# Kernel optimization log

Measured on AMD Instinct MI355X. Metric: run time of the kernel, lower is better.

The kernel has to match this reference:

```python
import jax, jax.numpy as jnp
import numpy as np

N_NODES = 100000
N_EDGES = 3200000
D_FEAT = 512
HIDDEN = 16
N_CLASSES = 7


def _gcn_conv(x, W, b, src, dst, n_nodes):
    """PyG GCNConv (add_self_loops=True, normalize=True):
    out = D^{-1/2} (A + I) D^{-1/2} X W + b, aggregated at target nodes (dst).
    src/dst already include self loops."""
    h = x @ W  # [N, out_dim] -- transform before scatter (small message dim)
    ones = jnp.ones(dst.shape[0], dtype=x.dtype)
    deg = jax.ops.segment_sum(ones, dst, num_segments=n_nodes)  # in-degree incl. self loop
    dinv = jnp.where(deg > 0, jax.lax.rsqrt(deg), 0.0)
    norm = dinv[src] * dinv[dst]  # [E_tot]
    msg = h[src] * norm[:, None]  # gather + scale
    out = jax.ops.segment_sum(msg, dst, num_segments=n_nodes)  # scatter-add
    return out + b


def setup_inputs() -> dict:
    key = jax.random.key(0)
    k1, k2, k3, k4 = jax.random.split(key, 4)
    x = jax.random.normal(k1, (N_NODES, D_FEAT), dtype=jnp.float32)
    edge_index = jax.random.randint(k2, (2, N_EDGES), 0, N_NODES, dtype=jnp.int64)
    # Glorot-ish init for weights
    W1 = jax.random.normal(k3, (D_FEAT, HIDDEN), dtype=jnp.float32) / np.sqrt(D_FEAT)
    b1 = jnp.zeros((HIDDEN,), dtype=jnp.float32)
    W2 = jax.random.normal(k4, (HIDDEN, N_CLASSES), dtype=jnp.float32) / np.sqrt(HIDDEN)
    b2 = jnp.zeros((N_CLASSES,), dtype=jnp.float32)
    return {"x": x, "edge_index": edge_index, "W1": W1, "b1": b1, "W2": W2, "b2": b2}


def reference(x, edge_index, W1, b1, W2, b2):
    n = x.shape[0]
    loop = jnp.arange(n, dtype=edge_index.dtype)
    src = jnp.concatenate([edge_index[0], loop])  # add self loops (fixed shape)
    dst = jnp.concatenate([edge_index[1], loop])
    h = _gcn_conv(x, W1, b1, src, dst, n)
    h = jax.nn.relu(h)
    # F.dropout(training=self.training): identity in eval/inference baseline
    h = _gcn_conv(h, W2, b2, src, dst, n)
    return jax.nn.log_softmax(h, axis=1)
```

## Files before the change

### kernel.cpp

```cpp
#include <hip/hip_runtime.h>

#define NN 100000
#define NE 3200000
#define DF 512
#define HID 16
#define NC 7
#define NBK 782
#define BCAP 6144
#define GEMM_BLOCKS 1563
#define SC_B 256

__global__ void k_zero_i(int* __restrict__ p, int n) {
    int i = blockIdx.x * blockDim.x + threadIdx.x;
    if (i < n) p[i] = 0;
}

__global__ __launch_bounds__(256) void k_fused(const float* __restrict__ x,
                                               const float* __restrict__ W1,
                                               const int* __restrict__ src,
                                               const int* __restrict__ dst,
                                               float* __restrict__ h1,
                                               int* __restrict__ bcnt,
                                               int* __restrict__ pk) {
    __shared__ float w[DF * HID];
    if (blockIdx.x >= GEMM_BLOCKS) {
        int* hist = (int*)w;
        int* cur  = hist + NBK;
        int b = blockIdx.x - GEMM_BLOCKS;
        const int per = (NE + SC_B - 1) / SC_B;
        int e0 = b * per;
        int e1 = min(e0 + per, NE);
        int tid = threadIdx.x;
        for (int i = tid; i < NBK; i += 256) hist[i] = 0;
        __syncthreads();
        for (int e = e0 + tid; e < e1; e += 256) atomicAdd(&hist[dst[e] >> 7], 1);
        __syncthreads();
        for (int i = tid; i < NBK; i += 256) cur[i] = atomicAdd(&bcnt[i], hist[i]);
        __syncthreads();
        for (int e = e0 + tid; e < e1; e += 256) {
            int d = dst[e];
            int bk = d >> 7;
            int pos = atomicAdd(&cur[bk], 1);
            if (pos < BCAP) pk[(size_t)bk * BCAP + pos] = src[e] | ((d & 127) << 17);
        }
        return;
    }
    {
        const float4* wg = (const float4*)W1;
        float4* wl = (float4*)w;
#pragma unroll
        for (int i = 0; i < 8; ++i) wl[threadIdx.x + 256 * i] = wg[threadIdx.x + 256 * i];
    }
    __syncthreads();
    int wid = (blockIdx.x * 256 + threadIdx.x) >> 6;
    int lane = threadIdx.x & 63;
    int r = lane >> 2, cc = lane & 3;
    int row = wid * 16 + r;
    if (row >= NN) return;
    const float4* xr = (const float4*)(x + (size_t)row * DF);
    const float4* wl = (const float4*)w;
    float4 acc = make_float4(0.f, 0.f, 0.f, 0.f);
#pragma unroll 4
    for (int i = 0; i < DF / 4; ++i) {
        float4 xv = xr[i];
        float4 w0 = wl[(4 * i + 0) * 4 + cc];
        float4 w1v = wl[(4 * i + 1) * 4 + cc];
        float4 w2 = wl[(4 * i + 2) * 4 + cc];
        float4 w3 = wl[(4 * i + 3) * 4 + cc];
        acc.x = fmaf(xv.x, w0.x, fmaf(xv.y, w1v.x, fmaf(xv.z, w2.x, fmaf(xv.w, w3.x, acc.x))));
        acc.y = fmaf(xv.x, w0.y, fmaf(xv.y, w1v.y, fmaf(xv.z, w2.y, fmaf(xv.w, w3.y, acc.y))));
        acc.z = fmaf(xv.x, w0.z, fmaf(xv.y, w1v.z, fmaf(xv.z, w2.z, fmaf(xv.w, w3.z, acc.z))));
        acc.w = fmaf(xv.x, w0.w, fmaf(xv.y, w1v.w, fmaf(xv.z, w2.w, fmaf(xv.w, w3.w, acc.w))));
    }
    *(float4*)(h1 + (size_t)row * HID + cc * 4) = acc;
}

__global__ __launch_bounds__(256) void k_sortB(const int* __restrict__ bcnt,
                                               int* __restrict__ pk,
                                               float* __restrict__ dinv,
                                               float* __restrict__ h1,
                                               int* __restrict__ ptrg,
                                               int* __restrict__ cntg) {
    __shared__ int sorted[BCAP];
    __shared__ int hist[128];
    __shared__ int off[128];
    __shared__ int cur[128];
    __shared__ float dl[128];
    int b = blockIdx.x, tid = threadIdx.x;
    if (tid < 128) hist[tid] = 0;
    __syncthreads();
    int n = min(bcnt[b], BCAP);
    int* p = pk + (size_t)b * BCAP;
    for (int i = tid; i < n; i += 256) atomicAdd(&hist[p[i] >> 17], 1);
    __syncthreads();
    if (tid < 128) off[tid] = hist[tid];
    __syncthreads();
    for (int s2 = 1; s2 < 128; s2 <<= 1) {
        int u = 0;
        if (tid < 128 && tid >= s2) u = off[tid - s2];
        __syncthreads();
        if (tid < 128) off[tid] += u;
        __syncthreads();
    }
    if (tid < 128) {
        int start = off[tid] - hist[tid];
        cur[tid] = start;
        int node = b * 128 + tid;
        float di = rsqrtf((float)hist[tid] + 1.0f);
        dl[tid] = di;
        if (node < NN) {
            dinv[node] = di;
            ptrg[node] = b * BCAP + start;
            cntg[node] = hist[tid];
        }
    }
    __syncthreads();
    for (int i = tid; i < n; i += 256) {
        int v = p[i];
        int pos = atomicAdd(&cur[v >> 17], 1);
        sorted[pos] = v & 0x1FFFF;
    }
    __syncthreads();
    for (int i = tid; i < n; i += 256) p[i] = sorted[i];
    float4* hp = (float4*)(h1 + (size_t)b * 128 * HID);
    for (int i = tid; i < 512; i += 256) {
        int ln = i >> 2;
        int node = b * 128 + ln;
        if (node < NN) {
            float di = dl[ln];
            float4 v = hp[i];
            v.x *= di; v.y *= di; v.z *= di; v.w *= di;
            hp[i] = v;
        }
    }
}

__global__ __launch_bounds__(256) void k_agg1(const int* __restrict__ ptrg,
                                              const int* __restrict__ cntg,
                                              const int* __restrict__ csr,
                                              const float* __restrict__ dinv,
                                              const float* __restrict__ h1s,
                                              const float* __restrict__ b1,
                                              const float* __restrict__ W2,
                                              float* __restrict__ h2s) {
    int tid = threadIdx.x;
    int ch = tid & 15;
    int d = blockIdx.x * 16 + (tid >> 4);
    if (d >= NN) return;
    int st = ptrg[d], n = cntg[d];
    float did = dinv[d];
    float a0 = 0.f, a1 = 0.f;
    int e = st, end = st + n;
    for (; e + 1 < end; e += 2) {
        int s0 = csr[e], s1 = csr[e + 1];
        a0 += h1s[(size_t)s0 * HID + ch];
        a1 += h1s[(size_t)s1 * HID + ch];
    }
    if (e < end) a0 += h1s[(size_t)csr[e] * HID + ch];
    float acc = (a0 + a1 + h1s[(size_t)d * HID + ch]) * did + b1[ch];
    float hr = fmaxf(acc, 0.f);
    float hj = 0.f;
#pragma unroll
    for (int k = 0; k < HID; ++k) {
        float hk = __shfl(hr, k, 16);
        if (ch < NC) hj = fmaf(hk, W2[k * NC + ch], hj);
    }
    if (ch < NC) h2s[(size_t)d * NC + ch] = hj * did;
}

__global__ __launch_bounds__(256) void k_agg2(const int* __restrict__ ptrg,
                                              const int* __restrict__ cntg,
                                              const int* __restrict__ csr,
                                              const float* __restrict__ dinv,
                                              const float* __restrict__ h2s,
                                              const float* __restrict__ b2,
                                              float* __restrict__ out) {
    int tid = threadIdx.x;
    int ch = tid & 7;
    int d = blockIdx.x * 32 + (tid >> 3);
    if (d >= NN) return;
    int st = ptrg[d], n = cntg[d];
    float did = dinv[d];
    float a0 = 0.f, a1 = 0.f;
    int e = st, end = st + n;
    for (; e + 1 < end; e += 2) {
        int s0 = csr[e], s1 = csr[e + 1];
        if (ch < NC) {
            a0 += h2s[(size_t)s0 * NC + ch];
            a1 += h2s[(size_t)s1 * NC + ch];
        }
    }
    if (e < end && ch < NC) a0 += h2s[(size_t)csr[e] * NC + ch];
    float o = -1e30f;
    if (ch < NC) o = (a0 + a1 + h2s[(size_t)d * NC + ch]) * did + b2[ch];
    float m = o;
#pragma unroll
    for (int offm = 1; offm < 8; offm <<= 1) m = fmaxf(m, __shfl_xor(m, offm, 8));
    float ex = (ch < NC) ? expf(o - m) : 0.f;
    float s8 = ex;
#pragma unroll
    for (int offm = 1; offm < 8; offm <<= 1) s8 += __shfl_xor(s8, offm, 8);
    if (ch < NC) out[(size_t)d * NC + ch] = o - m - logf(s8);
}

extern "C" void kernel_launch(void* const* d_in, const int* in_sizes, int n_in,
                              void* d_out, int out_size, void* d_ws, size_t ws_size,
                              hipStream_t stream) {
    const float* x  = (const float*)d_in[0];
    const int*   ei = (const int*)d_in[1];
    const float* W1 = (const float*)d_in[2];
    const float* b1 = (const float*)d_in[3];
    const float* W2 = (const float*)d_in[4];
    const float* b2 = (const float*)d_in[5];
    float* out = (float*)d_out;

    const int* src = ei;
    const int* dst = ei + NE;

    int*   bcnt = (int*)d_ws;
    int*   pk   = bcnt + 784;
    float* dinv = (float*)(pk + (size_t)NBK * BCAP);
    float* h1   = dinv + NN;
    float* h2   = h1 + (size_t)HID * NN;
    int*   ptrg = (int*)(h2 + (size_t)NC * NN);
    int*   cntg = ptrg + NN;

    k_zero_i<<<4, 256, 0, stream>>>(bcnt, 784);
    k_fused <<<GEMM_BLOCKS + SC_B, 256, 0, stream>>>(x, W1, src, dst, h1, bcnt, pk);
    k_sortB <<<NBK, 256, 0, stream>>>(bcnt, pk, dinv, h1, ptrg, cntg);
    k_agg1  <<<(NN + 15) / 16, 256, 0, stream>>>(ptrg, cntg, pk, dinv, h1, b1, W2, h2);
    k_agg2  <<<(NN + 31) / 32, 256, 0, stream>>>(ptrg, cntg, pk, dinv, h2, b2, out);
}
```

Before: 227.3 us.

## Stage bucket scatter in shared memory for coalesced writes, move scatter blocks first

The scatter blocks of the fused kernel now do a local counting sort of 5000 edges in LDS: a histogram, a block prefix scan, placement into a staging array, then a contiguous copy-out to each bucket using a binary search over the offsets. The goal is to replace the random per-edge global writes with mostly contiguous runs and to cut global atomics to one per non-empty bucket. Scatter blocks now sit at the front of the grid so they start early alongside the GEMM blocks, and there are more of them (640). The cost is extra LDS work, more barriers, and a binary search per element.

```diff
diff --git a/kernel.cpp b/kernel.cpp
--- a/kernel.cpp
+++ b/kernel.cpp
@@ -8,12 +8,24 @@
 #define NBK 782
 #define BCAP 6144
 #define GEMM_BLOCKS 1563
-#define SC_B 256
+#define SC_B 640
+#define SEDG 5000
 
 __global__ void k_zero_i(int* __restrict__ p, int n) {
     int i = blockIdx.x * blockDim.x + threadIdx.x;
     if (i < n) p[i] = 0;
 }
+
+union SMem {
+    float w[DF * HID];
+    struct {
+        int stage[SEDG];
+        int off[783];
+        int part[256];
+        int cur[782];
+        int gofs[782];
+    } s;
+};
 
 __global__ __launch_bounds__(256) void k_fused(const float* __restrict__ x,
                                                const float* __restrict__ W1,
@@ -22,43 +34,76 @@
                                                float* __restrict__ h1,
                                                int* __restrict__ bcnt,
                                                int* __restrict__ pk) {
-    __shared__ float w[DF * HID];
-    if (blockIdx.x >= GEMM_BLOCKS) {
-        int* hist = (int*)w;
-        int* cur  = hist + NBK;
-        int b = blockIdx.x - GEMM_BLOCKS;
-        const int per = (NE + SC_B - 1) / SC_B;
-        int e0 = b * per;
-        int e1 = min(e0 + per, NE);
-        int tid = threadIdx.x;
-        for (int i = tid; i < NBK; i += 256) hist[i] = 0;
-        __syncthreads();
-        for (int e = e0 + tid; e < e1; e += 256) atomicAdd(&hist[dst[e] >> 7], 1);
-        __syncthreads();
-        for (int i = tid; i < NBK; i += 256) cur[i] = atomicAdd(&bcnt[i], hist[i]);
-        __syncthreads();
-        for (int e = e0 + tid; e < e1; e += 256) {
+    __shared__ SMem u;
+    int tid = threadIdx.x;
+    if (blockIdx.x < SC_B) {
+        int* stage = u.s.stage;
+        int* off   = u.s.off;
+        int* part  = u.s.part;
+        int* cur   = u.s.cur;
+        int* gofs  = u.s.gofs;
+        int e0 = blockIdx.x * SEDG;
+        for (int i = tid; i < NBK; i += 256) cur[i] = 0;
+        __syncthreads();
+        for (int e = e0 + tid; e < e0 + SEDG; e += 256) atomicAdd(&cur[dst[e] >> 7], 1);
+        __syncthreads();
+        {
+            int base = tid * 4;
+            int sum = 0;
+#pragma unroll
+            for (int j = 0; j < 4; ++j) if (base + j < NBK) sum += cur[base + j];
+            part[tid] = sum;
+            __syncthreads();
+            for (int s2 = 1; s2 < 256; s2 <<= 1) {
+                int v = (tid >= s2) ? part[tid - s2] : 0;
+                __syncthreads();
+                part[tid] += v;
+                __syncthreads();
+            }
+            int run = (tid > 0) ? part[tid - 1] : 0;
+#pragma unroll
+            for (int j = 0; j < 4; ++j) {
+                int idx = base + j;
+                if (idx < NBK) { off[idx] = run; run += cur[idx]; }
+            }
+            if (tid == 0) off[NBK] = SEDG;
+        }
+        __syncthreads();
+        for (int i = tid; i < NBK; i += 256) {
+            int h = cur[i];
+            int g = h ? atomicAdd(&bcnt[i], h) : 0;
+            gofs[i] = g - off[i];
+            cur[i] = off[i];
+        }
+        __syncthreads();
+        for (int e = e0 + tid; e < e0 + SEDG; e += 256) {
             int d = dst[e];
-            int bk = d >> 7;
-            int pos = atomicAdd(&cur[bk], 1);
-            if (pos < BCAP) pk[(size_t)bk * BCAP + pos] = src[e] | ((d & 127) << 17);
+            int pos = atomicAdd(&cur[d >> 7], 1);
+            stage[pos] = src[e] | ((d & 127) << 17);
+        }
+        __syncthreads();
+        for (int i = tid; i < SEDG; i += 256) {
+            int lo = 0, hi = NBK;
+            while (hi - lo > 1) { int mid = (lo + hi) >> 1; if (off[mid] <= i) lo = mid; else hi = mid; }
+            int idx = gofs[lo] + i;
+            if (idx < BCAP) pk[(size_t)lo * BCAP + idx] = stage[i];
         }
         return;
     }
     {
         const float4* wg = (const float4*)W1;
-        float4* wl = (float4*)w;
-#pragma unroll
-        for (int i = 0; i < 8; ++i) wl[threadIdx.x + 256 * i] = wg[threadIdx.x + 256 * i];
-    }
-    __syncthreads();
-    int wid = (blockIdx.x * 256 + threadIdx.x) >> 6;
-    int lane = threadIdx.x & 63;
+        float4* wl = (float4*)u.w;
+#pragma unroll
+        for (int i = 0; i < 8; ++i) wl[tid + 256 * i] = wg[tid + 256 * i];
+    }
+    __syncthreads();
+    int wid = (blockIdx.x - SC_B) * 4 + (tid >> 6);
+    int lane = tid & 63;
     int r = lane >> 2, cc = lane & 3;
     int row = wid * 16 + r;
     if (row >= NN) return;
     const float4* xr = (const float4*)(x + (size_t)row * DF);
-    const float4* wl = (const float4*)w;
+    const float4* wl = (const float4*)u.w;
     float4 acc = make_float4(0.f, 0.f, 0.f, 0.f);
 #pragma unroll 4
     for (int i = 0; i < DF / 4; ++i) {
@@ -226,7 +271,7 @@
     int*   cntg = ptrg + NN;
 
     k_zero_i<<<4, 256, 0, stream>>>(bcnt, 784);
-    k_fused <<<GEMM_BLOCKS + SC_B, 256, 0, stream>>>(x, W1, src, dst, h1, bcnt, pk);
+    k_fused <<<SC_B + GEMM_BLOCKS, 256, 0, stream>>>(x, W1, src, dst, h1, bcnt, pk);
     k_sortB <<<NBK, 256, 0, stream>>>(bcnt, pk, dinv, h1, ptrg, cntg);
     k_agg1  <<<(NN + 15) / 16, 256, 0, stream>>>(ptrg, cntg, pk, dinv, h1, b1, W2, h2);
     k_agg2  <<<(NN + 31) / 32, 256, 0, stream>>>(ptrg, cntg, pk, dinv, h2, b2, out);
```

Result: faster. 197.8 us (-13.0%).
